# Kernel optimization log

Hardware: AMD Instinct MI355X
Metric: run time of the kernel (lower is better)

Reference implementation:

```python
import jax, jax.numpy as jnp
import numpy as np
from jax import lax

B, C, H, W = 16, 256, 64, 64
KNUM, KS, STRIDE, PAD, RED, GROUPS = 4, 3, 1, 1, 16, 4
BN_EPS = 1e-5


def setup_inputs() -> dict:
    key = jax.random.key(0)
    ks = jax.random.split(key, 12)
    f = jax.random.normal
    half, red = C // 2, C // RED
    return {
        "x": f(ks[0], (B, C, H, W), jnp.float32),
        "att_conv1d_w": f(ks[1], (3,), jnp.float32) * 0.5,                      # shared Conv1d(1,1,3) in Attention
        "att_out_w": f(ks[2], (C, C), jnp.float32) * (2.0 / C) ** 0.5,          # out_channel_conv2d 1x1
        "att_kernel_w": f(ks[3], (KNUM, C), jnp.float32) * (2.0 / C) ** 0.5,    # kernel_conv2d 1x1
        "ede_weight": f(ks[4], (KNUM, C, C, KS, KS), jnp.float32) * (2.0 / (C * KS * KS)) ** 0.5,
        "lga_conv1d_w": f(ks[5], (3,), jnp.float32) * 0.5,                      # LGA Conv1d(1,1,3) with bias
        "lga_conv1d_b": f(ks[6], (1,), jnp.float32) * 0.1,
        "lga_mlp_w1": f(ks[7], (red, half), jnp.float32) * (2.0 / half) ** 0.5,  # mlp conv 1x1 (no bias)
        "lga_mlp_w2": f(ks[8], (half, red), jnp.float32) * (2.0 / red) ** 0.5,
        "bn_gamma": jnp.ones((C,), jnp.float32),
        "bn_beta": jnp.zeros((C,), jnp.float32),
    }


def _conv1d_same(v_bc, w3):
    # 1-channel cross-correlation along the channel axis, pad=1 (PyTorch Conv1d)
    y = lax.conv_general_dilated(v_bc[:, None, :], w3[None, None, :], (1,), [(1, 1)],
                                 dimension_numbers=("NCH", "OIH", "NCH"))
    return y[:, 0, :]


def reference(x, att_conv1d_w, att_out_w, att_kernel_w, ede_weight,
              lga_conv1d_w, lga_conv1d_b, lga_mlp_w1, lga_mlp_w2,
              bn_gamma, bn_beta):
    b, c, h, w = x.shape

    # ---- EDE (Q branch): dynamic per-sample conv ----
    gap = x.mean(axis=(2, 3))                              # (b, c) global avg pool
    t = _conv1d_same(gap, att_conv1d_w)                    # shared conv1d over channels
    in_att = jax.nn.sigmoid(t)[:, :, None, None]           # (b, c, 1, 1)
    out_att = jax.nn.sigmoid(t @ att_out_w.T)[:, :, None, None]
    k_att = jax.nn.softmax(t @ att_kernel_w.T, axis=1)     # (b, KNUM)
    agg_w = jnp.einsum("bk,koipq->boipq", k_att, ede_weight)  # (b, C, C, KS, KS)
    x_mod = x * in_att

    def per_sample(xi, wi):  # xi: (C,H,W), wi: (C,C,KS,KS)
        return lax.conv_general_dilated(xi[None], wi, (STRIDE, STRIDE),
                                        [(PAD, PAD), (PAD, PAD)])[0]

    Q = jax.vmap(per_sample)(x_mod, agg_w) * out_att       # (b, C, H, W)

    # ---- LGA (K branch) ----
    half = c // 2
    in1, in2 = x[:, :half], x[:, half:]
    s = _conv1d_same(in1.mean(axis=(2, 3)), lga_conv1d_w) + lga_conv1d_b
    x1 = in1 * jax.nn.sigmoid(s)[:, :, None, None]

    def mlp(v):  # (b, half) -> (b, half); 1x1 convs on (b,half,1,1) == matmuls
        return jax.nn.relu(v @ lga_mlp_w1.T) @ lga_mlp_w2.T

    ch = jax.nn.sigmoid(mlp(in2.max(axis=(2, 3))) + mlp(in2.mean(axis=(2, 3))))
    y2 = in2 * ch[:, :, None, None]
    K = jnp.concatenate([x1, y2], axis=1)
    # channel shuffle with GROUPS groups
    K = K.reshape(b, GROUPS, c // GROUPS, h, w).transpose(0, 2, 1, 3, 4).reshape(b, c, h, w)

    # ---- fuse + BatchNorm (training-mode batch stats) + ReLU ----
    z = Q + K
    mean = z.mean(axis=(0, 2, 3))
    var = z.var(axis=(0, 2, 3))
    zn = (z - mean[None, :, None, None]) * lax.rsqrt(var[None, :, None, None] + BN_EPS)
    return jax.nn.relu(zn * bn_gamma[None, :, None, None] + bn_beta[None, :, None, None])
```

## Files before the change

### kernel.cpp

```cpp
#include <hip/hip_runtime.h>
#include <hip/hip_bf16.h>
#include <stdint.h>

#define HW_ 4096

typedef float f32x4 __attribute__((ext_vector_type(4)));
typedef short bf16x8 __attribute__((ext_vector_type(8)));

__device__ __forceinline__ unsigned short f2bf(float f) {
  __hip_bfloat16 h = __float2bfloat16(f);
  return *reinterpret_cast<unsigned short*>(&h);
}
__device__ __forceinline__ float sigmoidf_(float x) { return 1.f / (1.f + __expf(-x)); }

__device__ __forceinline__ void glds16(const void* g, void* l) {
  __builtin_amdgcn_global_load_lds(
      (const __attribute__((address_space(1))) unsigned int*)g,
      (__attribute__((address_space(3))) unsigned int*)l, 16, 0, 0);
}

__global__ void k_pre(const float* __restrict__ x, unsigned short* __restrict__ xtr,
                      float* __restrict__ psum, float* __restrict__ pmax) {
  int hwb = blockIdx.x;
  int cb = blockIdx.y;
  int b = blockIdx.z;
  int t = threadIdx.x;
  __shared__ float sv[64][65];
  int h16 = t & 15, g = t >> 4;
#pragma unroll
  for (int i = 0; i < 4; ++i) {
    int c_l = g + i * 16;
    float4 v = *reinterpret_cast<const float4*>(
        x + (((size_t)b * 256 + cb * 64 + c_l) << 12) + hwb * 64 + h16 * 4);
    *reinterpret_cast<float4*>(&sv[c_l][h16 * 4]) = v;
  }
  __syncthreads();
  {
    int c_l = t >> 2, q = t & 3;
    float s16 = 0.f, m16 = -3.4e38f;
#pragma unroll
    for (int j = 0; j < 16; ++j) {
      float vv = sv[c_l][q * 16 + j];
      s16 += vv; m16 = fmaxf(m16, vv);
    }
    s16 += __shfl_xor(s16, 1); s16 += __shfl_xor(s16, 2);
    m16 = fmaxf(m16, __shfl_xor(m16, 1)); m16 = fmaxf(m16, __shfl_xor(m16, 2));
    if (q == 0) {
      int c = cb * 64 + c_l;
      psum[(((size_t)b * 256 + c) << 6) + hwb] = s16;
      pmax[(((size_t)b * 256 + c) << 6) + hwb] = m16;
    }
  }
#pragma unroll
  for (int i = 0; i < 2; ++i) {
    int fp = t + i * 256;
    int hw2 = fp >> 3;
    int cp = (fp & 7) * 8;
    uint4 uu;
    uu.x = (unsigned)f2bf(sv[cp + 0][hw2]) | ((unsigned)f2bf(sv[cp + 1][hw2]) << 16);
    uu.y = (unsigned)f2bf(sv[cp + 2][hw2]) | ((unsigned)f2bf(sv[cp + 3][hw2]) << 16);
    uu.z = (unsigned)f2bf(sv[cp + 4][hw2]) | ((unsigned)f2bf(sv[cp + 5][hw2]) << 16);
    uu.w = (unsigned)f2bf(sv[cp + 6][hw2]) | ((unsigned)f2bf(sv[cp + 7][hw2]) << 16);
    *reinterpret_cast<uint4*>(xtr + (((size_t)b * 4096 + hwb * 64 + hw2) << 8) + cb * 64 + cp) = uu;
  }
}

__global__ void k_tiny(const float* __restrict__ psum, const float* __restrict__ pmax,
                       const float* __restrict__ aw3, const float* __restrict__ Wout,
                       const float* __restrict__ Wk, const float* __restrict__ lw3,
                       const float* __restrict__ lbia, const float* __restrict__ mw1,
                       const float* __restrict__ mw2,
                       float* __restrict__ in_att, float* __restrict__ out_att,
                       float* __restrict__ katt, float* __restrict__ sc,
                       float* __restrict__ sums, float* __restrict__ zerop) {
  int b = blockIdx.x, t = threadIdx.x;
  __shared__ float g[256], tt[256], red[256], hsum[16], ksm[4], mx[128];
  {
    const float4* pp = reinterpret_cast<const float4*>(psum + ((size_t)(b * 256 + t) << 6));
    const float4* pm = reinterpret_cast<const float4*>(pmax + ((size_t)(b * 256 + t) << 6));
    float s = 0.f, m = -3.4e38f;
#pragma unroll
    for (int j = 0; j < 16; ++j) {
      float4 a = pp[j]; s += (a.x + a.y) + (a.z + a.w);
      float4 q4 = pm[j];
      m = fmaxf(m, fmaxf(fmaxf(q4.x, q4.y), fmaxf(q4.z, q4.w)));
    }
    g[t] = s * (1.f / 4096.f);
    if (t >= 128) mx[t - 128] = m;
  }
  if (b == 0) {
    sums[t] = 0.f; sums[256 + t] = 0.f;
    zerop[t] = 0.f;
  }
  __syncthreads();
  float c0 = aw3[0], c1 = aw3[1], c2 = aw3[2];
  float tv = c1 * g[t];
  if (t > 0) tv += c0 * g[t - 1];
  if (t < 255) tv += c2 * g[t + 1];
  tt[t] = tv;
  in_att[b * 256 + t] = sigmoidf_(tv);
  __syncthreads();
  {
    float d = 0.f;
    const float4* wr = reinterpret_cast<const float4*>(Wout + (size_t)t * 256);
    for (int c4 = 0; c4 < 64; ++c4) {
      float4 wv4 = wr[c4];
      d += tt[c4 * 4] * wv4.x + tt[c4 * 4 + 1] * wv4.y + tt[c4 * 4 + 2] * wv4.z + tt[c4 * 4 + 3] * wv4.w;
    }
    out_att[b * 256 + t] = sigmoidf_(d);
  }
  int k = t >> 6, lane = t & 63;
  {
    float pk = 0.f;
    for (int c = lane; c < 256; c += 64) pk += tt[c] * Wk[k * 256 + c];
    red[t] = pk; __syncthreads();
    for (int off = 32; off > 0; off >>= 1) {
      if (lane < off) red[t] += red[t + off];
      __syncthreads();
    }
    if (t == 0) {
      float l0 = red[0], l1 = red[64], l2 = red[128], l3 = red[192];
      float mm = fmaxf(fmaxf(l0, l1), fmaxf(l2, l3));
      float e0 = __expf(l0 - mm), e1 = __expf(l1 - mm), e2 = __expf(l2 - mm), e3 = __expf(l3 - mm);
      float inv = 1.f / (e0 + e1 + e2 + e3);
      ksm[0] = e0 * inv; ksm[1] = e1 * inv; ksm[2] = e2 * inv; ksm[3] = e3 * inv;
    }
    __syncthreads();
    if (t < 4) katt[b * 4 + t] = ksm[t];
  }
  if (t < 128) {
    float a0 = lw3[0], a1 = lw3[1], a2 = lw3[2];
    float sv = a1 * g[t] + lbia[0];
    if (t > 0) sv += a0 * g[t - 1];
    if (t < 127) sv += a2 * g[t + 1];
    sc[b * 256 + t] = sigmoidf_(sv);
  }
  __syncthreads();
  if (t < 16) {
    float d1 = 0.f, d2 = 0.f;
    const float* w1r = mw1 + t * 128;
    for (int j = 0; j < 128; ++j) { d1 += mx[j] * w1r[j]; d2 += g[128 + j] * w1r[j]; }
    hsum[t] = fmaxf(d1, 0.f) + fmaxf(d2, 0.f);
  }
  __syncthreads();
  if (t < 128) {
    float dd = 0.f;
    const float* w2r = mw2 + t * 16;
    for (int r = 0; r < 16; ++r) dd += hsum[r] * w2r[r];
    sc[b * 256 + 128 + t] = sigmoidf_(dd);
  }
}

__global__ __launch_bounds__(256) void k_agg(const float* __restrict__ ede,
                                             const float* __restrict__ katt,
                                             const float* __restrict__ inatt,
                                             unsigned short* __restrict__ agg) {
  __shared__ float eds[4][2304];
  int o = blockIdx.x, t = threadIdx.x;
#pragma unroll
  for (int k = 0; k < 4; ++k) {
    const float* src = ede + ((size_t)k * 256 + o) * 2304;
#pragma unroll
    for (int j = 0; j < 9; ++j) eds[k][j * 256 + t] = src[j * 256 + t];
  }
  __syncthreads();
  int ii = (t & 127) * 2;
  int bh = t >> 7;
  int fg = o >> 4, r = o & 15;
  int cs = ii >> 5, lh = (ii >> 3) & 3, jj = ii & 7;
  for (int b2 = 0; b2 < 8; ++b2) {
    int b = b2 * 2 + bh;
    float k0 = katt[b * 4], k1 = katt[b * 4 + 1], k2 = katt[b * 4 + 2], k3 = katt[b * 4 + 3];
    float ia0 = inatt[b * 256 + ii], ia1 = inatt[b * 256 + ii + 1];
#pragma unroll
    for (int pq = 0; pq < 9; ++pq) {
      float v0 = k0 * eds[0][ii * 9 + pq] + k1 * eds[1][ii * 9 + pq] +
                 k2 * eds[2][ii * 9 + pq] + k3 * eds[3][ii * 9 + pq];
      float v1 = k0 * eds[0][(ii + 1) * 9 + pq] + k1 * eds[1][(ii + 1) * 9 + pq] +
                 k2 * eds[2][(ii + 1) * 9 + pq] + k3 * eds[3][(ii + 1) * 9 + pq];
      v0 *= ia0; v1 *= ia1;
      unsigned int u = (unsigned)f2bf(v0) | ((unsigned)f2bf(v1) << 16);
      size_t base = (((((size_t)(b * 9 + pq) * 8 + cs) * 16 + fg) * 64 + lh * 16 + r) << 3) + jj;
      *reinterpret_cast<unsigned int*>(agg + base) = u;
    }
  }
}

__global__ __launch_bounds__(512, 4) void k_conv(
    const unsigned short* __restrict__ agg, const unsigned short* __restrict__ xtr,
    const float* __restrict__ x, const float* __restrict__ oatt,
    const float* __restrict__ sc, const float* __restrict__ zerop,
    float* __restrict__ sums, float* __restrict__ zout) {
  __shared__ __align__(16) char smem[49152];
  int wg = blockIdx.x;
  int bswz = ((wg & 7) << 6) | (wg >> 3);
  int b = bswz >> 5;
  int ot = (bswz >> 4) & 1;
  int pt = bswz & 15;
  int tid = threadIdx.x;
  int l = tid & 63;
  int wv = tid >> 6;
  int wm = wv >> 2, wn = wv & 3;
  int w0 = l & 15, ks = l >> 4;
  bool maskl0 = (w0 == 0), maskl15 = (w0 == 15);

  auto slabsrc = [&](int j) -> const char* {
    int idx = j * 512 + tid;
    int P = idx >> 2, sp = idx & 3;
    int sr = P >> 6, w = P & 63;
    int imgrow = pt * 4 + sr - 1;
    int ir = imgrow < 0 ? 0 : (imgrow > 63 ? 63 : imgrow);
    int slog = sp ^ ((w >> 1) & 3);
    const char* gp = (const char*)(xtr + (((size_t)b * 4096 + ir * 64 + w) << 8) + slog * 8);
    return ((unsigned)imgrow < 64u) ? gp : (const char*)zerop;
  };
  const char* sb0_ = slabsrc(0);
  const char* sb1_ = slabsrc(1);
  const char* sb2_ = slabsrc(2);

  auto aP = [&](int pq, int cs, int fm) -> const unsigned short* {
    return agg + ((((size_t)(b * 9 + pq) * 8 + cs) * 16 + ot * 8 + wm * 4 + fm) << 9) + l * 8;
  };

  f32x4 acc[4][4];
  f32x4 zero4 = {0.f, 0.f, 0.f, 0.f};
#pragma unroll
  for (int i2 = 0; i2 < 4; ++i2)
#pragma unroll
    for (int j2 = 0; j2 < 4; ++j2) acc[i2][j2] = zero4;

  bf16x8 z8 = {0, 0, 0, 0, 0, 0, 0, 0};

  {
    char* sd = smem;
    glds16(sb0_, sd + tid * 16);
    glds16(sb1_, sd + 8192 + tid * 16);
    glds16(sb2_, sd + 16384 + tid * 16);
  }
  asm volatile("s_waitcnt vmcnt(0)" ::: "memory");
  __builtin_amdgcn_s_barrier();

  for (int c = 0; c < 8; ++c) {
    const char* sb = smem + ((c & 1) ? 24576 : 0);
    if (c < 7) {
      char* sd = smem + (((c + 1) & 1) ? 24576 : 0);
      glds16(sb0_ + (c + 1) * 64, sd + tid * 16);
      glds16(sb1_ + (c + 1) * 64, sd + 8192 + tid * 16);
      glds16(sb2_ + (c + 1) * 64, sd + 16384 + tid * 16);
    }
#pragma unroll
    for (int pq = 0; pq < 9; ++pq) {
      const int dp = pq / 3, dq = pq % 3;
      bf16x8 af[4];
#pragma unroll
      for (int fm = 0; fm < 4; ++fm)
        af[fm] = *reinterpret_cast<const bf16x8*>(aP(pq, c, fm));
      bf16x8 bv[4];
      int rowb = (wn + dp) << 6;
#pragma unroll
      for (int fn = 0; fn < 4; ++fn) {
        int wcol = w0 + fn * 16 + (dq - 1);
        int wc = wcol < 0 ? 0 : (wcol > 63 ? 63 : wcol);
        int bo = ((rowb + wc) << 6) + ((ks ^ ((wc >> 1) & 3)) << 4);
        bv[fn] = *reinterpret_cast<const bf16x8*>(sb + bo);
      }
      if (dq == 0) bv[0] = maskl0 ? z8 : bv[0];
      if (dq == 2) bv[3] = maskl15 ? z8 : bv[3];
      __builtin_amdgcn_s_setprio(1);
#pragma unroll
      for (int fm = 0; fm < 4; ++fm)
#pragma unroll
        for (int fn = 0; fn < 4; ++fn)
          acc[fm][fn] = __builtin_amdgcn_mfma_f32_16x16x32_bf16(af[fm], bv[fn], acc[fm][fn], 0, 0, 0);
      __builtin_amdgcn_s_setprio(0);
    }
    asm volatile("s_waitcnt vmcnt(0)" ::: "memory");
    __builtin_amdgcn_s_barrier();
  }
  __syncthreads();

  float* ls = (float*)smem;
  if (tid < 256) ls[tid] = 0.f;
  __syncthreads();

#pragma unroll
  for (int fm = 0; fm < 4; ++fm) {
#pragma unroll
    for (int r = 0; r < 4; ++r) {
      int ml = wm * 64 + fm * 16 + ((l >> 4) << 2) + r;
      int gm = ot * 128 + ml;
      int oc = ((gm & 3) << 6) | (gm >> 2);
      float oav = oatt[b * 256 + gm];
      float scv = sc[b * 256 + oc];
      const float* xrow = x + (((size_t)b * 256 + oc) << 12) + pt * 256;
      float* zrow = zout + (((size_t)b * 256 + gm) << 12) + pt * 256;
      float psv = 0.f, psv2 = 0.f;
#pragma unroll
      for (int fn = 0; fn < 4; ++fn) {
        int n = wn * 64 + fn * 16 + (l & 15);
        float zv = acc[fm][fn][r] * oav + xrow[n] * scv;
        zrow[n] = zv;
        psv += zv; psv2 += zv * zv;
      }
#pragma unroll
      for (int d = 8; d > 0; d >>= 1) {
        psv += __shfl_down(psv, d, 16);
        psv2 += __shfl_down(psv2, d, 16);
      }
      if ((l & 15) == 0) {
        atomicAdd(&ls[ml], psv);
        atomicAdd(&ls[128 + ml], psv2);
      }
    }
  }
  __syncthreads();
  if (tid < 128) {
    atomicAdd(&sums[ot * 128 + tid], ls[tid]);
    atomicAdd(&sums[256 + ot * 128 + tid], ls[128 + tid]);
  }
}

__global__ void k_apply(float* __restrict__ z, const float* __restrict__ sums,
                        const float* __restrict__ gamma, const float* __restrict__ beta) {
  int idx = blockIdx.x * 256 + threadIdx.x;
  for (int i = idx; i < 4194304; i += 4096 * 256) {
    int c = (i >> 10) & 255;
    float mean = sums[c] * (1.f / 65536.f);
    float var = sums[256 + c] * (1.f / 65536.f) - mean * mean;
    float scale = gamma[c] * rsqrtf(var + 1e-5f);
    float shift = beta[c] - mean * scale;
    float4* p = reinterpret_cast<float4*>(z) + i;
    float4 v = *p;
    v.x = fmaxf(v.x * scale + shift, 0.f);
    v.y = fmaxf(v.y * scale + shift, 0.f);
    v.z = fmaxf(v.z * scale + shift, 0.f);
    v.w = fmaxf(v.w * scale + shift, 0.f);
    *p = v;
  }
}

extern "C" void kernel_launch(void* const* d_in, const int* in_sizes, int n_in,
                              void* d_out, int out_size, void* d_ws, size_t ws_size,
                              hipStream_t stream) {
  (void)in_sizes; (void)n_in; (void)out_size; (void)ws_size;
  const float* x = (const float*)d_in[0];
  const float* aw3 = (const float*)d_in[1];
  const float* Wout = (const float*)d_in[2];
  const float* Wk = (const float*)d_in[3];
  const float* ede = (const float*)d_in[4];
  const float* lw3 = (const float*)d_in[5];
  const float* lbia = (const float*)d_in[6];
  const float* mw1 = (const float*)d_in[7];
  const float* mw2 = (const float*)d_in[8];
  const float* gamma = (const float*)d_in[9];
  const float* beta = (const float*)d_in[10];

  char* ws = (char*)d_ws;
  float* inatt = (float*)(ws + 32768);
  float* oatt  = (float*)(ws + 49152);
  float* katt  = (float*)(ws + 65536);
  float* sc    = (float*)(ws + 65792);
  float* zerop = (float*)(ws + 82176);
  float* sums  = (float*)(ws + 83200);
  unsigned short* xtr = (unsigned short*)(ws + 262144);
  unsigned short* agg = (unsigned short*)(ws + 262144 + 33554432);
  float* psum = (float*)(ws + 262144 + 33554432);
  float* pmax = (float*)(ws + 262144 + 33554432 + 1048576);
  float* z = (float*)d_out;

  k_pre<<<dim3(64, 4, 16), 256, 0, stream>>>(x, xtr, psum, pmax);
  k_tiny<<<16, 256, 0, stream>>>(psum, pmax, aw3, Wout, Wk, lw3, lbia, mw1, mw2,
                                 inatt, oatt, katt, sc, sums, zerop);
  k_agg<<<256, 256, 0, stream>>>(ede, katt, inatt, agg);
  k_conv<<<512, 512, 0, stream>>>(agg, xtr, x, oatt, sc, zerop, sums, z);
  k_apply<<<4096, 256, 0, stream>>>(z, sums, gamma, beta);
}
```

Measured before the change: 156.5 us.

## Stage dynamic weights through LDS and retile conv to full 256 output channels

The aggregated weights now use a plain row-major [b][o][pq][i] layout and are staged through LDS, double-buffered, with global_load_lds and an XOR swizzle. Each conv workgroup now covers all 256 output channels for a 2-row pixel tile, where before it covered 128 channels for a 4-row tile. The aim is to remove per-fragment global loads of weights, halve redundant input-slab loads across output-channel tiles, and simplify the agg write pattern. In exchange, LDS use grows to 64KB, which may cut occupancy, and a vmcnt wait plus barrier now runs after every pq step instead of once per channel chunk.

Result: slower. 164.2 us (+4.9%).

```diff
diff --git a/kernel.cpp b/kernel.cpp
--- a/kernel.cpp
+++ b/kernel.cpp
@@ -166,12 +166,11 @@
   __syncthreads();
   int ii = (t & 127) * 2;
   int bh = t >> 7;
-  int fg = o >> 4, r = o & 15;
-  int cs = ii >> 5, lh = (ii >> 3) & 3, jj = ii & 7;
   for (int b2 = 0; b2 < 8; ++b2) {
     int b = b2 * 2 + bh;
     float k0 = katt[b * 4], k1 = katt[b * 4 + 1], k2 = katt[b * 4 + 2], k3 = katt[b * 4 + 3];
     float ia0 = inatt[b * 256 + ii], ia1 = inatt[b * 256 + ii + 1];
+    size_t obase = ((size_t)(b * 256 + o) * 9) << 8;
 #pragma unroll
     for (int pq = 0; pq < 9; ++pq) {
       float v0 = k0 * eds[0][ii * 9 + pq] + k1 * eds[1][ii * 9 + pq] +
@@ -180,8 +179,7 @@
                  k2 * eds[2][(ii + 1) * 9 + pq] + k3 * eds[3][(ii + 1) * 9 + pq];
       v0 *= ia0; v1 *= ia1;
       unsigned int u = (unsigned)f2bf(v0) | ((unsigned)f2bf(v1) << 16);
-      size_t base = (((((size_t)(b * 9 + pq) * 8 + cs) * 16 + fg) * 64 + lh * 16 + r) << 3) + jj;
-      *reinterpret_cast<unsigned int*>(agg + base) = u;
+      *reinterpret_cast<unsigned int*>(agg + obase + (pq << 8) + ii) = u;
     }
   }
 }
@@ -191,24 +189,30 @@
     const float* __restrict__ x, const float* __restrict__ oatt,
     const float* __restrict__ sc, const float* __restrict__ zerop,
     float* __restrict__ sums, float* __restrict__ zout) {
-  __shared__ __align__(16) char smem[49152];
+  __shared__ __align__(16) char smem[65536];
   int wg = blockIdx.x;
   int bswz = ((wg & 7) << 6) | (wg >> 3);
   int b = bswz >> 5;
-  int ot = (bswz >> 4) & 1;
-  int pt = bswz & 15;
+  int pt = bswz & 31;
   int tid = threadIdx.x;
   int l = tid & 63;
   int wv = tid >> 6;
-  int wm = wv >> 2, wn = wv & 3;
+  int wm = wv >> 1, wn = wv & 1;
   int w0 = l & 15, ks = l >> 4;
   bool maskl0 = (w0 == 0), maskl15 = (w0 == 15);
+
+  int r0 = tid >> 2, s0 = tid & 3;
+  int r1 = r0 + 128;
+  int f0 = (s0 ^ ((r0 >> 1) & 3)) << 3;
+  int f1 = (s0 ^ ((r1 >> 1) & 3)) << 3;
+  const unsigned short* aS0 = agg + (size_t)(b * 256 + r0) * 2304 + f0;
+  const unsigned short* aS1 = agg + (size_t)(b * 256 + r1) * 2304 + f1;
 
   auto slabsrc = [&](int j) -> const char* {
     int idx = j * 512 + tid;
     int P = idx >> 2, sp = idx & 3;
     int sr = P >> 6, w = P & 63;
-    int imgrow = pt * 4 + sr - 1;
+    int imgrow = pt * 2 + sr - 1;
     int ir = imgrow < 0 ? 0 : (imgrow > 63 ? 63 : imgrow);
     int slog = sp ^ ((w >> 1) & 3);
     const char* gp = (const char*)(xtr + (((size_t)b * 4096 + ir * 64 + w) << 8) + slog * 8);
@@ -216,11 +220,13 @@
   };
   const char* sb0_ = slabsrc(0);
   const char* sb1_ = slabsrc(1);
-  const char* sb2_ = slabsrc(2);
-
-  auto aP = [&](int pq, int cs, int fm) -> const unsigned short* {
-    return agg + ((((size_t)(b * 9 + pq) * 8 + cs) * 16 + ot * 8 + wm * 4 + fm) << 9) + l * 8;
-  };
+
+  int aOff[4];
+#pragma unroll
+  for (int fm = 0; fm < 4; ++fm) {
+    int R = wm * 64 + fm * 16 + (l & 15);
+    aOff[fm] = R * 64 + (((l >> 4) ^ ((R >> 1) & 3)) << 4);
+  }
 
   f32x4 acc[4][4];
   f32x4 zero4 = {0.f, 0.f, 0.f, 0.f};
@@ -231,31 +237,37 @@
 
   bf16x8 z8 = {0, 0, 0, 0, 0, 0, 0, 0};
 
-  {
-    char* sd = smem;
-    glds16(sb0_, sd + tid * 16);
-    glds16(sb1_, sd + 8192 + tid * 16);
-    glds16(sb2_, sd + 16384 + tid * 16);
-  }
+#define ASTG(NPQ, NC, BUF)                                               \
+  { char* ad_ = smem + (BUF) * 16384;                                    \
+    glds16(aS0 + (NPQ) * 256 + (NC) * 32, ad_ + tid * 16);               \
+    glds16(aS1 + (NPQ) * 256 + (NC) * 32, ad_ + 8192 + tid * 16); }
+
+#define SLSTG(CN)                                                        \
+  { char* sd_ = smem + 32768 + (((CN) & 1) ? 16384 : 0);                 \
+    glds16(sb0_ + (CN) * 64, sd_ + tid * 16);                            \
+    glds16(sb1_ + (CN) * 64, sd_ + 8192 + tid * 16); }
+
+  SLSTG(0);
+  ASTG(0, 0, 0);
   asm volatile("s_waitcnt vmcnt(0)" ::: "memory");
   __builtin_amdgcn_s_barrier();
 
   for (int c = 0; c < 8; ++c) {
-    const char* sb = smem + ((c & 1) ? 24576 : 0);
-    if (c < 7) {
-      char* sd = smem + (((c + 1) & 1) ? 24576 : 0);
-      glds16(sb0_ + (c + 1) * 64, sd + tid * 16);
-      glds16(sb1_ + (c + 1) * 64, sd + 8192 + tid * 16);
-      glds16(sb2_ + (c + 1) * 64, sd + 16384 + tid * 16);
-    }
+    const char* sb = smem + 32768 + ((c & 1) ? 16384 : 0);
 #pragma unroll
     for (int pq = 0; pq < 9; ++pq) {
+      int t = c * 9 + pq;
+      if (t < 71) {
+        int npq = (pq < 8) ? pq + 1 : 0;
+        int nc = (pq < 8) ? c : c + 1;
+        ASTG(npq, nc, (t + 1) & 1);
+      }
+      if (pq == 6 && c < 7) SLSTG(c + 1);
+      const char* ab = smem + (t & 1) * 16384;
       const int dp = pq / 3, dq = pq % 3;
-      bf16x8 af[4];
-#pragma unroll
-      for (int fm = 0; fm < 4; ++fm)
-        af[fm] = *reinterpret_cast<const bf16x8*>(aP(pq, c, fm));
-      bf16x8 bv[4];
+      bf16x8 af[4], bv[4];
+#pragma unroll
+      for (int f = 0; f < 4; ++f) af[f] = *reinterpret_cast<const bf16x8*>(ab + aOff[f]);
       int rowb = (wn + dp) << 6;
 #pragma unroll
       for (int fn = 0; fn < 4; ++fn) {
@@ -273,27 +285,26 @@
         for (int fn = 0; fn < 4; ++fn)
           acc[fm][fn] = __builtin_amdgcn_mfma_f32_16x16x32_bf16(af[fm], bv[fn], acc[fm][fn], 0, 0, 0);
       __builtin_amdgcn_s_setprio(0);
-    }
-    asm volatile("s_waitcnt vmcnt(0)" ::: "memory");
-    __builtin_amdgcn_s_barrier();
+      asm volatile("s_waitcnt vmcnt(0)" ::: "memory");
+      __builtin_amdgcn_s_barrier();
+    }
   }
   __syncthreads();
 
   float* ls = (float*)smem;
-  if (tid < 256) ls[tid] = 0.f;
+  if (tid < 512) { ls[tid] = 0.f; }
   __syncthreads();
 
 #pragma unroll
   for (int fm = 0; fm < 4; ++fm) {
 #pragma unroll
     for (int r = 0; r < 4; ++r) {
-      int ml = wm * 64 + fm * 16 + ((l >> 4) << 2) + r;
-      int gm = ot * 128 + ml;
-      int oc = ((gm & 3) << 6) | (gm >> 2);
-      float oav = oatt[b * 256 + gm];
+      int m = wm * 64 + fm * 16 + ((l >> 4) << 2) + r;
+      int oc = ((m & 3) << 6) | (m >> 2);
+      float oav = oatt[b * 256 + m];
       float scv = sc[b * 256 + oc];
-      const float* xrow = x + (((size_t)b * 256 + oc) << 12) + pt * 256;
-      float* zrow = zout + (((size_t)b * 256 + gm) << 12) + pt * 256;
+      const float* xrow = x + (((size_t)b * 256 + oc) << 12) + pt * 128;
+      float* zrow = zout + (((size_t)b * 256 + m) << 12) + pt * 128;
       float psv = 0.f, psv2 = 0.f;
 #pragma unroll
       for (int fn = 0; fn < 4; ++fn) {
@@ -308,15 +319,15 @@
         psv2 += __shfl_down(psv2, d, 16);
       }
       if ((l & 15) == 0) {
-        atomicAdd(&ls[ml], psv);
-        atomicAdd(&ls[128 + ml], psv2);
-      }
-    }
-  }
-  __syncthreads();
-  if (tid < 128) {
-    atomicAdd(&sums[ot * 128 + tid], ls[tid]);
-    atomicAdd(&sums[256 + ot * 128 + tid], ls[128 + tid]);
+        atomicAdd(&ls[m], psv);
+        atomicAdd(&ls[256 + m], psv2);
+      }
+    }
+  }
+  __syncthreads();
+  if (tid < 256) {
+    atomicAdd(&sums[tid], ls[tid]);
+    atomicAdd(&sums[256 + tid], ls[256 + tid]);
   }
 }
 
```
